# Performance work log

Hardware: AMD Instinct MI355X
Metric: run time of the kernel (lower is better)

Reference implementation:

```python
import jax, jax.numpy as jnp
import numpy as np
from jax import lax

B, L = 2, 5000            # images, candidate lines per image
C_IN, C_LOI = 256, 128    # backbone channels, dim_loi
H = W = 256               # feature-map spatial size (indices clamped to 255)
N_PTS0, N_PTS1 = 32, 8    # points sampled per line, after maxpool
POOL = N_PTS0 // N_PTS1   # MaxPool1d kernel/stride = 4
PLANES = C_LOI // 2       # Bottleneck1D mid channels
EPS = 1e-5


def setup_inputs() -> dict:
    key = jax.random.key(0)
    ks = jax.random.split(key, 16)
    f32 = jnp.float32
    s = 0.05
    feature = jax.random.normal(ks[0], (B, C_IN, H, W), f32)
    lines = jax.random.uniform(ks[1], (B, L, 2, 2), f32, minval=0.0, maxval=255.0)
    return {
        "feature": feature,
        "lines": lines,
        "fc1_w": jax.random.normal(ks[2], (C_LOI, C_IN), f32) * s,
        "fc1_b": jnp.zeros((C_LOI,), f32),
        "bn1_g": jnp.ones((C_LOI,), f32),
        "bn1_b": jnp.zeros((C_LOI,), f32),
        "bn1_m": jax.random.normal(ks[3], (C_LOI,), f32) * 0.1,
        "bn1_v": jax.random.uniform(ks[4], (C_LOI,), f32, minval=0.5, maxval=1.5),
        "conv1_w": jax.random.normal(ks[5], (PLANES, C_LOI), f32) * s,
        "conv1_b": jnp.zeros((PLANES,), f32),
        "bn2_g": jnp.ones((PLANES,), f32),
        "bn2_b": jnp.zeros((PLANES,), f32),
        "bn2_m": jax.random.normal(ks[6], (PLANES,), f32) * 0.1,
        "bn2_v": jax.random.uniform(ks[7], (PLANES,), f32, minval=0.5, maxval=1.5),
        "conv2_w": jax.random.normal(ks[8], (PLANES, PLANES, 3), f32) * s,
        "conv2_b": jnp.zeros((PLANES,), f32),
        "bn3_g": jnp.ones((PLANES,), f32),
        "bn3_b": jnp.zeros((PLANES,), f32),
        "bn3_m": jax.random.normal(ks[9], (PLANES,), f32) * 0.1,
        "bn3_v": jax.random.uniform(ks[10], (PLANES,), f32, minval=0.5, maxval=1.5),
        "conv3_w": jax.random.normal(ks[11], (C_LOI, PLANES), f32) * s,
        "conv3_b": jnp.zeros((C_LOI,), f32),
        "fc2_w": jax.random.normal(ks[12], (3, C_LOI * N_PTS1), f32) * s,
        "fc2_b": jnp.zeros((3,), f32),
    }


def _bn(x, g, b, m, v):
    # eval-mode BatchNorm1d over [N, C, T]
    inv = g / jnp.sqrt(v + EPS)
    return x * inv[None, :, None] + (b - m * inv)[None, :, None]


def _bilinear_sample(feat, lines):
    # feat: [B, C, H, W], lines: [B, L, 2, 2] -> [B, L, C, N_PTS0]
    lam = jnp.linspace(0.0, 1.0, N_PTS0, dtype=feat.dtype)[:, None]  # [P,1]
    # p = lam * endpoint0 + (1-lam) * endpoint1 - 0.5  -> [B, L, P, 2]
    p = lines[:, :, 0:1, :] * lam + lines[:, :, 1:2, :] * (1.0 - lam) - 0.5
    px, py = p[..., 0], p[..., 1]                       # [B, L, P]
    px0 = jnp.clip(jnp.floor(px), 0.0, 255.0)
    py0 = jnp.clip(jnp.floor(py), 0.0, 255.0)
    px1 = jnp.clip(px0 + 1.0, 0.0, 255.0)
    py1 = jnp.clip(py0 + 1.0, 0.0, 255.0)
    ix0, iy0 = px0.astype(jnp.int32), py0.astype(jnp.int32)
    ix1, iy1 = px1.astype(jnp.int32), py1.astype(jnp.int32)
    w00 = (px1 - px) * (py1 - py)
    w10 = (px - px0) * (py1 - py)
    w01 = (px1 - px) * (py - py0)
    w11 = (px - px0) * (py - py0)

    def one_image(f, a0, b0, a1, b1, c00, c10, c01, c11):
        # f: [C,H,W], indices/weights: [L,P] -> [C,L,P]
        return (f[:, a0, b0] * c00 + f[:, a1, b0] * c10 +
                f[:, a0, b1] * c01 + f[:, a1, b1] * c11)

    xp = jax.vmap(one_image)(feat, ix0, iy0, ix1, iy1, w00, w10, w01, w11)
    return jnp.transpose(xp, (0, 2, 1, 3))  # [B, L, C, P]


def _forward(feature, lines, fc1_w, fc1_b, bn1_g, bn1_b, bn1_m, bn1_v,
             conv1_w, conv1_b, bn2_g, bn2_b, bn2_m, bn2_v,
             conv2_w, conv2_b, bn3_g, bn3_b, bn3_m, bn3_v,
             conv3_w, conv3_b, fc2_w, fc2_b):
    # fc1: 1x1 conv over the backbone feature map
    x = jnp.einsum('oc,bchw->bohw', fc1_w, feature) + fc1_b[None, :, None, None]
    xp = _bilinear_sample(x, lines)                     # [B, L, C_LOI, P]
    xp = xp.reshape(B * L, C_LOI, N_PTS0)
    # MaxPool1d(kernel=POOL, stride=POOL)
    xp = xp.reshape(B * L, C_LOI, N_PTS1, POOL).max(axis=-1)  # [N, C, T]
    # Bottleneck1D residual branch: BN-ReLU-Conv1(k1)-BN-ReLU-Conv(k3)-BN-ReLU-Conv(k1)
    h = jax.nn.relu(_bn(xp, bn1_g, bn1_b, bn1_m, bn1_v))
    h = jnp.einsum('oc,nct->not', conv1_w, h) + conv1_b[None, :, None]
    h = jax.nn.relu(_bn(h, bn2_g, bn2_b, bn2_m, bn2_v))
    h = lax.conv_general_dilated(h, conv2_w, window_strides=(1,),
                                 padding=((1, 1),),
                                 dimension_numbers=('NCH', 'OIH', 'NCH'))
    h = h + conv2_b[None, :, None]
    h = jax.nn.relu(_bn(h, bn3_g, bn3_b, bn3_m, bn3_v))
    h = jnp.einsum('oc,nct->not', conv3_w, h) + conv3_b[None, :, None]
    xp = xp + h
    # fc2: ReLU + Linear(dim_loi * n_pts1 -> 3)
    flat = jax.nn.relu(xp).reshape(B * L, C_LOI * N_PTS1)
    return flat @ fc2_w.T + fc2_b


def reference(feature, lines, fc1_w, fc1_b, bn1_g, bn1_b, bn1_m, bn1_v,
              conv1_w, conv1_b, bn2_g, bn2_b, bn2_m, bn2_v,
              conv2_w, conv2_b, bn3_g, bn3_b, bn3_m, bn3_v,
              conv3_w, conv3_b, fc2_w, fc2_b):
    return _forward(feature, lines, fc1_w, fc1_b, bn1_g, bn1_b, bn1_m, bn1_v,
                    conv1_w, conv1_b, bn2_g, bn2_b, bn2_m, bn2_v,
                    conv2_w, conv2_b, bn3_g, bn3_b, bn3_m, bn3_v,
                    conv3_w, conv3_b, fc2_w, fc2_b)
```

## Files before the change

### kernel.cpp

```cpp
#include <hip/hip_runtime.h>
#include <hip/hip_bf16.h>

#define BB 2
#define LL 5000
#define CIN 256
#define CLOI 128
#define HH 256
#define WW 256
#define HWP (HH*WW)
#define NPTS0 32
#define NPTS1 8
#define PLANES 64
#define EPSV 1e-5f

#define X_BYTES   ((size_t)BB * HWP * CLOI * 2)
#define XS_BYTES  ((size_t)BB * LL * 1024 * 2)
#define W1S_OFF   (X_BYTES + XS_BYTES)
#define W2S_OFF   (W1S_OFF + 16384)
#define W3S_OFF   (W2S_OFF + 24576)
#define B1P_OFF   (W3S_OFF + 16384)
#define B2P_OFF   (B1P_OFF + 256)
#define S1_OFF    (B2P_OFF + 256)
#define T1_OFF    (S1_OFF + 512)
#define W0S_OFF   (T1_OFF + 512)

typedef unsigned int uint;
typedef unsigned short ushort;
typedef __attribute__((ext_vector_type(8))) short short8;
typedef __attribute__((ext_vector_type(4))) float f32x4;

__device__ __forceinline__ float bf2f(ushort u) {
    uint v = ((uint)u) << 16;
    return __uint_as_float(v);
}
__device__ __forceinline__ ushort f2bf(float f) {
    uint x = __float_as_uint(f);
    uint r = (x + 0x7fffu + ((x >> 16) & 1u)) >> 16;
    return (ushort)r;
}
__device__ __forceinline__ uint pack2(float a, float b) {
    return (uint)f2bf(a) | ((uint)f2bf(b) << 16);
}

__global__ __launch_bounds__(256) void fc1_kernel(
    const float* __restrict__ feature, const ushort* __restrict__ w0s,
    const float* __restrict__ fc1_b, ushort* __restrict__ xout)
{
    __shared__ ushort sF[32 * 64 * 8];

    int tid = threadIdx.x;
    int tile = blockIdx.x;
    int b = tile >> 10;
    int p0 = (tile & 1023) << 6;
    int wv = tid >> 6, lane = tid & 63;
    int q = lane >> 4, ln = lane & 15;

    short8 afr[8][2];
#pragma unroll
    for (int kg = 0; kg < 8; kg++)
#pragma unroll
        for (int mt = 0; mt < 2; mt++)
            afr[kg][mt] = *(const short8*)(w0s + ((size_t)((kg * 4 + q) * 128 + wv * 32 + mt * 16 + ln)) * 8);

    const float* fb = feature + (size_t)b * CIN * HWP + p0;
    int g_ = tid >> 4;
    int qd = tid & 15;
#pragma unroll
    for (int s = 0; s < 2; s++) {
        int g = s * 16 + g_;
        const float* src = fb + (size_t)(g * 8) * HWP + qd * 4;
        float4 rv[8];
#pragma unroll
        for (int j = 0; j < 8; j++) rv[j] = *(const float4*)(src + (size_t)j * HWP);
#pragma unroll
        for (int i = 0; i < 4; i++) {
            uint4 u;
            u.x = pack2(((const float*)&rv[0])[i], ((const float*)&rv[1])[i]);
            u.y = pack2(((const float*)&rv[2])[i], ((const float*)&rv[3])[i]);
            u.z = pack2(((const float*)&rv[4])[i], ((const float*)&rv[5])[i]);
            u.w = pack2(((const float*)&rv[6])[i], ((const float*)&rv[7])[i]);
            *(uint4*)(&sF[(g * 64 + qd * 4 + i) * 8]) = u;
        }
    }
    __syncthreads();

    const f32x4 fzero = { 0.f, 0.f, 0.f, 0.f };
    f32x4 acc[2][4];
#pragma unroll
    for (int mt = 0; mt < 2; mt++)
#pragma unroll
        for (int nt = 0; nt < 4; nt++) acc[mt][nt] = fzero;

#pragma unroll
    for (int kg = 0; kg < 8; kg++) {
#pragma unroll
        for (int nt = 0; nt < 4; nt++) {
            short8 bfr = *(short8*)(&sF[((kg * 4 + q) * 64 + nt * 16 + ln) * 8]);
            acc[0][nt] = __builtin_amdgcn_mfma_f32_16x16x32_bf16(afr[kg][0], bfr, acc[0][nt], 0, 0, 0);
            acc[1][nt] = __builtin_amdgcn_mfma_f32_16x16x32_bf16(afr[kg][1], bfr, acc[1][nt], 0, 0, 0);
        }
    }

    float bias[8];
    *(float4*)bias       = *(const float4*)(fc1_b + wv * 32 + q * 4);
    *(float4*)(bias + 4) = *(const float4*)(fc1_b + wv * 32 + 16 + q * 4);
    ushort* xrow = xout + (size_t)b * HWP * CLOI;
#pragma unroll
    for (int mt = 0; mt < 2; mt++)
#pragma unroll
        for (int nt = 0; nt < 4; nt++) {
            uint2 u;
            u.x = pack2(acc[mt][nt][0] + bias[mt * 4 + 0], acc[mt][nt][1] + bias[mt * 4 + 1]);
            u.y = pack2(acc[mt][nt][2] + bias[mt * 4 + 2], acc[mt][nt][3] + bias[mt * 4 + 3]);
            *(uint2*)(xrow + (size_t)(p0 + nt * 16 + ln) * CLOI + wv * 32 + mt * 16 + q * 4) = u;
        }
}

__global__ __launch_bounds__(256) void prep_kernel(
    const float* __restrict__ conv1_w, const float* __restrict__ conv1_b,
    const float* __restrict__ bn2_g, const float* __restrict__ bn2_b,
    const float* __restrict__ bn2_m, const float* __restrict__ bn2_v,
    const float* __restrict__ conv2_w, const float* __restrict__ conv2_b,
    const float* __restrict__ bn3_g, const float* __restrict__ bn3_b,
    const float* __restrict__ bn3_m, const float* __restrict__ bn3_v,
    const float* __restrict__ conv3_w,
    const float* __restrict__ bn1_g, const float* __restrict__ bn1_b,
    const float* __restrict__ bn1_m, const float* __restrict__ bn1_v,
    const float* __restrict__ fc1_w,
    ushort* __restrict__ w1s, ushort* __restrict__ w2s, ushort* __restrict__ w3s,
    float* __restrict__ b1p, float* __restrict__ b2p,
    float* __restrict__ s1o, float* __restrict__ t1o,
    ushort* __restrict__ w0s)
{
    int idx = blockIdx.x * 256 + threadIdx.x;
    if (idx < 8192) {
        int kg = idx >> 9, rem = idx & 511, m = rem >> 3, j = rem & 7;
        int c = kg * 8 + j;
        float s2 = bn2_g[m] * rsqrtf(bn2_v[m] + EPSV);
        w1s[idx] = f2bf(conv1_w[m * 128 + c] * s2);
    }
    if (idx < 12288) {
        int dt = idx >> 12, rem = idx & 4095;
        int kg = rem >> 9, m = (rem >> 3) & 63, j = rem & 7;
        int i = kg * 8 + j;
        float s3 = bn3_g[m] * rsqrtf(bn3_v[m] + EPSV);
        w2s[idx] = f2bf(conv2_w[m * 192 + i * 3 + dt] * s3);
    }
    if (idx < 8192) {
        int kg = idx >> 10, rem = idx & 1023, m = rem >> 3, j = rem & 7;
        w3s[idx] = f2bf(conv3_w[m * 64 + kg * 8 + j]);
    }
    if (idx < 32768) {
        int grp = idx >> 10, rem = idx & 1023, m = rem >> 3, j = rem & 7;
        w0s[idx] = f2bf(fc1_w[m * CIN + grp * 8 + j]);
    }
    if (idx < 64) {
        float s2 = bn2_g[idx] * rsqrtf(bn2_v[idx] + EPSV);
        b1p[idx] = conv1_b[idx] * s2 + bn2_b[idx] - bn2_m[idx] * s2;
        float s3 = bn3_g[idx] * rsqrtf(bn3_v[idx] + EPSV);
        b2p[idx] = conv2_b[idx] * s3 + bn3_b[idx] - bn3_m[idx] * s3;
    }
    if (idx < 128) {
        float s1 = bn1_g[idx] * rsqrtf(bn1_v[idx] + EPSV);
        s1o[idx] = s1;
        t1o[idx] = bn1_b[idx] - bn1_m[idx] * s1;
    }
}

__global__ __launch_bounds__(256, 4) void sample_head_kernel(
    const ushort* __restrict__ x, const float* __restrict__ lines,
    const ushort* __restrict__ w1s, const ushort* __restrict__ w2s,
    const ushort* __restrict__ w3s,
    const float* __restrict__ b1p, const float* __restrict__ b2p,
    const float* __restrict__ s1g, const float* __restrict__ t1g,
    const float* __restrict__ conv3_b,
    const float* __restrict__ fc2_w, const float* __restrict__ fc2_b,
    float* __restrict__ out)
{
    __shared__ ushort sH1[8192];
    __shared__ ushort sB2[4096];
    __shared__ int   sIdx[8][32][4];
    __shared__ float sWt[8][32][4];
    __shared__ float sB1[64], sB2b[64], sB3b[128];

    int tid = threadIdx.x;
    int wv = tid >> 6, lane = tid & 63;
    int q = lane >> 4, ln = lane & 15;
    int L0 = blockIdx.x * 8;
    int b = L0 / LL;
    int colg = wv * 16 + ln;

    if (tid < 128) sB3b[tid] = conv3_b[tid];
    if (tid < 64)  { sB1[tid] = b1p[tid]; sB2b[tid] = b2p[tid]; }

    float s1a = s1g[2 * lane], s1c = s1g[2 * lane + 1];
    float t1a = t1g[2 * lane], t1c = t1g[2 * lane + 1];

    {
        int l = tid >> 5, j = tid & 31;
        float lam = (float)j * (1.0f / 31.0f);
        const float* lp = lines + (size_t)(L0 + l) * 4;
        float e0x = lp[0], e0y = lp[1], e1x = lp[2], e1y = lp[3];
        float px = e0x * lam + e1x * (1.f - lam) - 0.5f;
        float py = e0y * lam + e1y * (1.f - lam) - 0.5f;
        float px0 = fminf(fmaxf(floorf(px), 0.f), 255.f);
        float py0 = fminf(fmaxf(floorf(py), 0.f), 255.f);
        float px1 = fminf(px0 + 1.f, 255.f);
        float py1 = fminf(py0 + 1.f, 255.f);
        int ix0 = (int)px0, iy0 = (int)py0, ix1 = (int)px1, iy1 = (int)py1;
        sIdx[l][j][0] = ix0 * WW + iy0;
        sIdx[l][j][1] = ix1 * WW + iy0;
        sIdx[l][j][2] = ix0 * WW + iy1;
        sIdx[l][j][3] = ix1 * WW + iy1;
        sWt[l][j][0] = (px1 - px) * (py1 - py);
        sWt[l][j][1] = (px - px0) * (py1 - py);
        sWt[l][j][2] = (px1 - px) * (py - py0);
        sWt[l][j][3] = (px - px0) * (py - py0);
    }
    __syncthreads();

    const uint* xb = (const uint*)(x + (size_t)b * HWP * CLOI);
    int kg = lane >> 2;
    int j2 = (lane & 3) * 2;
    int swz = (kg & 7) << 3;

    uint xsu[8][2];
#pragma unroll
    for (int l = 0; l < 8; l++) {
        float m00 = -INFINITY, m10 = -INFINITY;
        float m01 = -INFINITY, m11 = -INFINITY;
#pragma unroll
        for (int jj = 0; jj < 8; jj++) {
            int j = wv * 8 + jj;
            int4   iv = *(const int4*)(&sIdx[l][j][0]);
            float4 wvv = *(const float4*)(&sWt[l][j][0]);
            uint u00 = xb[(size_t)iv.x * 64 + lane];
            uint u10 = xb[(size_t)iv.y * 64 + lane];
            uint u01 = xb[(size_t)iv.z * 64 + lane];
            uint u11 = xb[(size_t)iv.w * 64 + lane];
            float v0 = bf2f((ushort)(u00 & 0xffff)) * wvv.x + bf2f((ushort)(u10 & 0xffff)) * wvv.y
                     + bf2f((ushort)(u01 & 0xffff)) * wvv.z + bf2f((ushort)(u11 & 0xffff)) * wvv.w;
            float v1 = bf2f((ushort)(u00 >> 16)) * wvv.x + bf2f((ushort)(u10 >> 16)) * wvv.y
                     + bf2f((ushort)(u01 >> 16)) * wvv.z + bf2f((ushort)(u11 >> 16)) * wvv.w;
            if (jj < 4) { m00 = fmaxf(m00, v0); m10 = fmaxf(m10, v1); }
            else        { m01 = fmaxf(m01, v0); m11 = fmaxf(m11, v1); }
        }
        xsu[l][0] = pack2(m00, m10);
        xsu[l][1] = pack2(m01, m11);
        int col0 = l * 8 + 2 * wv;
        int base0 = (kg * 64 + col0) * 8 + j2;
        float h00 = fmaxf(m00 * s1a + t1a, 0.f), h10 = fmaxf(m10 * s1c + t1c, 0.f);
        float h01 = fmaxf(m01 * s1a + t1a, 0.f), h11 = fmaxf(m11 * s1c + t1c, 0.f);
        *(uint*)(&sH1[base0 ^ swz])       = pack2(h00, h10);
        *(uint*)(&sH1[(base0 + 8) ^ swz]) = pack2(h01, h11);
    }
    __syncthreads();

    const short8 bzero = { 0, 0, 0, 0, 0, 0, 0, 0 };
    const f32x4 fzero = { 0.f, 0.f, 0.f, 0.f };

    f32x4 acc1[4];
#pragma unroll
    for (int mt = 0; mt < 4; mt++) acc1[mt] = fzero;
#pragma unroll
    for (int ks = 0; ks < 4; ks++) {
        int kk = ks * 4 + q;
        short8 bfrag = *(short8*)(&sH1[((kk * 64 + colg) * 8) ^ ((kk & 7) << 3)]);
#pragma unroll
        for (int mt = 0; mt < 4; mt++) {
            short8 a = *(const short8*)(w1s + (kk * 64 + mt * 16 + ln) * 8);
            acc1[mt] = __builtin_amdgcn_mfma_f32_16x16x32_bf16(a, bfrag, acc1[mt], 0, 0, 0);
        }
    }
#pragma unroll
    for (int mt = 0; mt < 4; mt++) {
        int m0 = mt * 16 + q * 4;
        float v0 = fmaxf(acc1[mt][0] + sB1[m0 + 0], 0.f);
        float v1 = fmaxf(acc1[mt][1] + sB1[m0 + 1], 0.f);
        float v2 = fmaxf(acc1[mt][2] + sB1[m0 + 2], 0.f);
        float v3 = fmaxf(acc1[mt][3] + sB1[m0 + 3], 0.f);
        uint2 u; u.x = pack2(v0, v1); u.y = pack2(v2, v3);
        *(uint2*)(&sB2[((m0 >> 3) * 64 + colg) * 8 + (m0 & 7)]) = u;
    }
    __syncthreads();

#pragma unroll
    for (int l = 0; l < 8; l++) {
        int col0 = l * 8 + 2 * wv;
        int base0 = (kg * 64 + col0) * 8 + j2;
        *(uint*)(&sH1[base0 ^ swz])       = xsu[l][0];
        *(uint*)(&sH1[(base0 + 8) ^ swz]) = xsu[l][1];
    }

    int tpos = colg & 7;
    short8 bfr2[3][2];
#pragma unroll
    for (int dt = 0; dt < 3; dt++) {
        int tsh = tpos + dt - 1;
        bool valid = ((unsigned)tsh < 8u);
        int colr = colg + dt - 1;
        colr = colr < 0 ? 0 : (colr > 63 ? 63 : colr);
#pragma unroll
        for (int ks = 0; ks < 2; ks++) {
            short8 bfrag = *(short8*)(&sB2[((ks * 4 + q) * 64 + colr) * 8]);
            bfr2[dt][ks] = valid ? bfrag : bzero;
        }
    }
    __syncthreads();

    f32x4 acc2[4];
#pragma unroll
    for (int mt = 0; mt < 4; mt++) acc2[mt] = fzero;
#pragma unroll
    for (int dt = 0; dt < 3; dt++)
#pragma unroll
        for (int ks = 0; ks < 2; ks++) {
            int kk = ks * 4 + q;
#pragma unroll
            for (int mt = 0; mt < 4; mt++) {
                short8 a = *(const short8*)(w2s + dt * 4096 + (kk * 64 + mt * 16 + ln) * 8);
                acc2[mt] = __builtin_amdgcn_mfma_f32_16x16x32_bf16(a, bfr2[dt][ks], acc2[mt], 0, 0, 0);
            }
        }
#pragma unroll
    for (int mt = 0; mt < 4; mt++) {
        int m0 = mt * 16 + q * 4;
        float v0 = fmaxf(acc2[mt][0] + sB2b[m0 + 0], 0.f);
        float v1 = fmaxf(acc2[mt][1] + sB2b[m0 + 1], 0.f);
        float v2 = fmaxf(acc2[mt][2] + sB2b[m0 + 2], 0.f);
        float v3 = fmaxf(acc2[mt][3] + sB2b[m0 + 3], 0.f);
        uint2 u; u.x = pack2(v0, v1); u.y = pack2(v2, v3);
        *(uint2*)(&sB2[((m0 >> 3) * 64 + colg) * 8 + (m0 & 7)]) = u;
    }
    __syncthreads();

    f32x4 acc3[8];
#pragma unroll
    for (int mt = 0; mt < 8; mt++) acc3[mt] = fzero;
#pragma unroll
    for (int ks = 0; ks < 2; ks++) {
        int kk = ks * 4 + q;
        short8 bfrag = *(short8*)(&sB2[(kk * 64 + colg) * 8]);
#pragma unroll
        for (int mt = 0; mt < 8; mt++) {
            short8 a = *(const short8*)(w3s + (kk * 128 + mt * 16 + ln) * 8);
            acc3[mt] = __builtin_amdgcn_mfma_f32_16x16x32_bf16(a, bfrag, acc3[mt], 0, 0, 0);
        }
    }

    float p0 = 0.f, p1 = 0.f, p2 = 0.f;
#pragma unroll
    for (int mt = 0; mt < 8; mt++) {
#pragma unroll
        for (int r = 0; r < 4; r++) {
            int m = mt * 16 + q * 4 + r;
            int idx = ((m >> 3) * 512 + colg * 8 + (m & 7)) ^ (((m >> 3) & 7) << 3);
            float xsv = bf2f(sH1[idx]);
            float v = fmaxf(xsv + acc3[mt][r] + sB3b[m], 0.f);
            int fi = m * 8 + tpos;
            p0 += v * fc2_w[fi];
            p1 += v * fc2_w[1024 + fi];
            p2 += v * fc2_w[2048 + fi];
        }
    }
    p0 += __shfl_xor(p0, 32); p1 += __shfl_xor(p1, 32); p2 += __shfl_xor(p2, 32);
    p0 += __shfl_xor(p0, 16); p1 += __shfl_xor(p1, 16); p2 += __shfl_xor(p2, 16);
    p0 += __shfl_xor(p0, 4);  p1 += __shfl_xor(p1, 4);  p2 += __shfl_xor(p2, 4);
    p0 += __shfl_xor(p0, 2);  p1 += __shfl_xor(p1, 2);  p2 += __shfl_xor(p2, 2);
    p0 += __shfl_xor(p0, 1);  p1 += __shfl_xor(p1, 1);  p2 += __shfl_xor(p2, 1);

    if (lane == 0 || lane == 8) {
        int line = L0 + wv * 2 + (lane >> 3);
        out[(size_t)line * 3 + 0] = p0 + fc2_b[0];
        out[(size_t)line * 3 + 1] = p1 + fc2_b[1];
        out[(size_t)line * 3 + 2] = p2 + fc2_b[2];
    }
}

extern "C" void kernel_launch(void* const* d_in, const int* in_sizes, int n_in,
                              void* d_out, int out_size, void* d_ws, size_t ws_size,
                              hipStream_t stream) {
    const float* feature = (const float*)d_in[0];
    const float* lines   = (const float*)d_in[1];
    const float* fc1_w   = (const float*)d_in[2];
    const float* fc1_b   = (const float*)d_in[3];
    const float* bn1_g   = (const float*)d_in[4];
    const float* bn1_b   = (const float*)d_in[5];
    const float* bn1_m   = (const float*)d_in[6];
    const float* bn1_v   = (const float*)d_in[7];
    const float* conv1_w = (const float*)d_in[8];
    const float* conv1_b = (const float*)d_in[9];
    const float* bn2_g   = (const float*)d_in[10];
    const float* bn2_b   = (const float*)d_in[11];
    const float* bn2_m   = (const float*)d_in[12];
    const float* bn2_v   = (const float*)d_in[13];
    const float* conv2_w = (const float*)d_in[14];
    const float* conv2_b = (const float*)d_in[15];
    const float* bn3_g   = (const float*)d_in[16];
    const float* bn3_b   = (const float*)d_in[17];
    const float* bn3_m   = (const float*)d_in[18];
    const float* bn3_v   = (const float*)d_in[19];
    const float* conv3_w = (const float*)d_in[20];
    const float* conv3_b = (const float*)d_in[21];
    const float* fc2_w   = (const float*)d_in[22];
    const float* fc2_b   = (const float*)d_in[23];
    float* out = (float*)d_out;

    char* ws = (char*)d_ws;
    ushort* x_bf = (ushort*)ws;
    ushort* w1s  = (ushort*)(ws + W1S_OFF);
    ushort* w2s  = (ushort*)(ws + W2S_OFF);
    ushort* w3s  = (ushort*)(ws + W3S_OFF);
    float*  b1p  = (float*)(ws + B1P_OFF);
    float*  b2p  = (float*)(ws + B2P_OFF);
    float*  s1g  = (float*)(ws + S1_OFF);
    float*  t1g  = (float*)(ws + T1_OFF);
    ushort* w0s  = (ushort*)(ws + W0S_OFF);

    prep_kernel<<<128, 256, 0, stream>>>(
        conv1_w, conv1_b, bn2_g, bn2_b, bn2_m, bn2_v,
        conv2_w, conv2_b, bn3_g, bn3_b, bn3_m, bn3_v,
        conv3_w, bn1_g, bn1_b, bn1_m, bn1_v, fc1_w,
        w1s, w2s, w3s, b1p, b2p, s1g, t1g, w0s);
    fc1_kernel<<<2048, 256, 0, stream>>>(feature, w0s, fc1_b, x_bf);
    sample_head_kernel<<<BB * LL / 8, 256, 0, stream>>>(
        x_bf, lines, w1s, w2s, w3s, b1p, b2p, s1g, t1g, conv3_b, fc2_w, fc2_b, out);
}
```

Measured before the change: 298.3 us.

## Alias shared buffers, raise occupancy, and batch gather loads per half-window

The sample-index and weight shared arrays now share one 8 KB buffer with the later sB2 scratch, which cuts LDS use per block. Launch bounds go from 4 to 6 blocks per SM. The gather loop issues all 16 global loads for a 4-point pooling window before doing the math, so more memory requests are in flight. The risks are register pressure under the tighter occupancy bound, possible spills, and needing a barrier before sB2 reuses the aliased region.

```diff
diff --git a/kernel.cpp b/kernel.cpp
--- a/kernel.cpp
+++ b/kernel.cpp
@@ -167,7 +167,7 @@
     }
 }
 
-__global__ __launch_bounds__(256, 4) void sample_head_kernel(
+__global__ __launch_bounds__(256, 6) void sample_head_kernel(
     const ushort* __restrict__ x, const float* __restrict__ lines,
     const ushort* __restrict__ w1s, const ushort* __restrict__ w2s,
     const ushort* __restrict__ w3s,
@@ -178,10 +178,12 @@
     float* __restrict__ out)
 {
     __shared__ ushort sH1[8192];
-    __shared__ ushort sB2[4096];
-    __shared__ int   sIdx[8][32][4];
-    __shared__ float sWt[8][32][4];
+    __shared__ __align__(16) char sU[8192];
     __shared__ float sB1[64], sB2b[64], sB3b[128];
+
+    int4*   sIdx = (int4*)sU;
+    float4* sWt  = (float4*)(sU + 4096);
+    ushort* sB2  = (ushort*)sU;
 
     int tid = threadIdx.x;
     int wv = tid >> 6, lane = tid & 63;
@@ -208,14 +210,17 @@
         float px1 = fminf(px0 + 1.f, 255.f);
         float py1 = fminf(py0 + 1.f, 255.f);
         int ix0 = (int)px0, iy0 = (int)py0, ix1 = (int)px1, iy1 = (int)py1;
-        sIdx[l][j][0] = ix0 * WW + iy0;
-        sIdx[l][j][1] = ix1 * WW + iy0;
-        sIdx[l][j][2] = ix0 * WW + iy1;
-        sIdx[l][j][3] = ix1 * WW + iy1;
-        sWt[l][j][0] = (px1 - px) * (py1 - py);
-        sWt[l][j][1] = (px - px0) * (py1 - py);
-        sWt[l][j][2] = (px1 - px) * (py - py0);
-        sWt[l][j][3] = (px - px0) * (py - py0);
+        int4 iv; float4 wt;
+        iv.x = ix0 * WW + iy0;
+        iv.y = ix1 * WW + iy0;
+        iv.z = ix0 * WW + iy1;
+        iv.w = ix1 * WW + iy1;
+        wt.x = (px1 - px) * (py1 - py);
+        wt.y = (px - px0) * (py1 - py);
+        wt.z = (px1 - px) * (py - py0);
+        wt.w = (px - px0) * (py - py0);
+        sIdx[l * 32 + j] = iv;
+        sWt[l * 32 + j]  = wt;
     }
     __syncthreads();
 
@@ -227,32 +232,41 @@
     uint xsu[8][2];
 #pragma unroll
     for (int l = 0; l < 8; l++) {
-        float m00 = -INFINITY, m10 = -INFINITY;
-        float m01 = -INFINITY, m11 = -INFINITY;
-#pragma unroll
-        for (int jj = 0; jj < 8; jj++) {
-            int j = wv * 8 + jj;
-            int4   iv = *(const int4*)(&sIdx[l][j][0]);
-            float4 wvv = *(const float4*)(&sWt[l][j][0]);
-            uint u00 = xb[(size_t)iv.x * 64 + lane];
-            uint u10 = xb[(size_t)iv.y * 64 + lane];
-            uint u01 = xb[(size_t)iv.z * 64 + lane];
-            uint u11 = xb[(size_t)iv.w * 64 + lane];
-            float v0 = bf2f((ushort)(u00 & 0xffff)) * wvv.x + bf2f((ushort)(u10 & 0xffff)) * wvv.y
-                     + bf2f((ushort)(u01 & 0xffff)) * wvv.z + bf2f((ushort)(u11 & 0xffff)) * wvv.w;
-            float v1 = bf2f((ushort)(u00 >> 16)) * wvv.x + bf2f((ushort)(u10 >> 16)) * wvv.y
-                     + bf2f((ushort)(u01 >> 16)) * wvv.z + bf2f((ushort)(u11 >> 16)) * wvv.w;
-            if (jj < 4) { m00 = fmaxf(m00, v0); m10 = fmaxf(m10, v1); }
-            else        { m01 = fmaxf(m01, v0); m11 = fmaxf(m11, v1); }
-        }
-        xsu[l][0] = pack2(m00, m10);
-        xsu[l][1] = pack2(m01, m11);
-        int col0 = l * 8 + 2 * wv;
-        int base0 = (kg * 64 + col0) * 8 + j2;
-        float h00 = fmaxf(m00 * s1a + t1a, 0.f), h10 = fmaxf(m10 * s1c + t1c, 0.f);
-        float h01 = fmaxf(m01 * s1a + t1a, 0.f), h11 = fmaxf(m11 * s1c + t1c, 0.f);
-        *(uint*)(&sH1[base0 ^ swz])       = pack2(h00, h10);
-        *(uint*)(&sH1[(base0 + 8) ^ swz]) = pack2(h01, h11);
+        float mA0, mA1;
+#pragma unroll
+        for (int jh = 0; jh < 2; jh++) {
+            uint u[4][4];
+#pragma unroll
+            for (int jj = 0; jj < 4; jj++) {
+                int4 iv = sIdx[l * 32 + wv * 8 + jh * 4 + jj];
+                u[jj][0] = xb[(size_t)iv.x * 64 + lane];
+                u[jj][1] = xb[(size_t)iv.y * 64 + lane];
+                u[jj][2] = xb[(size_t)iv.z * 64 + lane];
+                u[jj][3] = xb[(size_t)iv.w * 64 + lane];
+            }
+            float m0 = -INFINITY, m1 = -INFINITY;
+#pragma unroll
+            for (int jj = 0; jj < 4; jj++) {
+                float4 wt = sWt[l * 32 + wv * 8 + jh * 4 + jj];
+                float v0 = bf2f((ushort)(u[jj][0] & 0xffff)) * wt.x + bf2f((ushort)(u[jj][1] & 0xffff)) * wt.y
+                         + bf2f((ushort)(u[jj][2] & 0xffff)) * wt.z + bf2f((ushort)(u[jj][3] & 0xffff)) * wt.w;
+                float v1 = bf2f((ushort)(u[jj][0] >> 16)) * wt.x + bf2f((ushort)(u[jj][1] >> 16)) * wt.y
+                         + bf2f((ushort)(u[jj][2] >> 16)) * wt.z + bf2f((ushort)(u[jj][3] >> 16)) * wt.w;
+                m0 = fmaxf(m0, v0);
+                m1 = fmaxf(m1, v1);
+            }
+            if (jh == 0) { mA0 = m0; mA1 = m1; }
+            else {
+                xsu[l][0] = pack2(mA0, mA1);
+                xsu[l][1] = pack2(m0, m1);
+                int col0 = l * 8 + 2 * wv;
+                int base0 = (kg * 64 + col0) * 8 + j2;
+                float h00 = fmaxf(mA0 * s1a + t1a, 0.f), h10 = fmaxf(mA1 * s1c + t1c, 0.f);
+                float h01 = fmaxf(m0 * s1a + t1a, 0.f),  h11 = fmaxf(m1 * s1c + t1c, 0.f);
+                *(uint*)(&sH1[base0 ^ swz])       = pack2(h00, h10);
+                *(uint*)(&sH1[(base0 + 8) ^ swz]) = pack2(h01, h11);
+            }
+        }
     }
     __syncthreads();
 
```

Result: slower. 310.4 us (+4.1%).

## Widen bilinear gather loads, compress sample metadata, alias LDS for higher occupancy

Applied to the files above, without the earlier changes.

The bilinear gather is restructured. Each lane now loads four bf16 channels (uint2), and each half-wave handles one sample point. All 16 corner loads are issued before any math, to expose more memory-level parallelism. Per-point metadata shrinks to one base index plus two weights, with the other corners derived by fixed offsets. The index and weight scratch now share LDS with sB2, and launch bounds rise from 4 to 5 blocks per SM to raise occupancy. The cost is higher register pressure, and the upper-edge clamp is dropped: a base coordinate of 255 would read the wrong or out-of-range neighbour.

```diff
diff --git a/kernel.cpp b/kernel.cpp
--- a/kernel.cpp
+++ b/kernel.cpp
@@ -167,7 +167,7 @@
     }
 }
 
-__global__ __launch_bounds__(256, 4) void sample_head_kernel(
+__global__ __launch_bounds__(256, 5) void sample_head_kernel(
     const ushort* __restrict__ x, const float* __restrict__ lines,
     const ushort* __restrict__ w1s, const ushort* __restrict__ w2s,
     const ushort* __restrict__ w3s,
@@ -178,10 +178,12 @@
     float* __restrict__ out)
 {
     __shared__ ushort sH1[8192];
-    __shared__ ushort sB2[4096];
-    __shared__ int   sIdx[8][32][4];
-    __shared__ float sWt[8][32][4];
+    __shared__ __align__(16) char sU[8192];
     __shared__ float sB1[64], sB2b[64], sB3b[128];
+
+    int*    sI  = (int*)sU;
+    float2* sW2 = (float2*)(sU + 1024);
+    ushort* sB2 = (ushort*)sU;
 
     int tid = threadIdx.x;
     int wv = tid >> 6, lane = tid & 63;
@@ -193,8 +195,13 @@
     if (tid < 128) sB3b[tid] = conv3_b[tid];
     if (tid < 64)  { sB1[tid] = b1p[tid]; sB2b[tid] = b2p[tid]; }
 
-    float s1a = s1g[2 * lane], s1c = s1g[2 * lane + 1];
-    float t1a = t1g[2 * lane], t1c = t1g[2 * lane + 1];
+    int half = lane >> 5;
+    int lc = lane & 31;
+    int kg = lc >> 1, j4 = (lc & 1) * 4;
+    int swz = (kg & 7) << 3;
+
+    float4 s1v = *(const float4*)(s1g + lc * 4);
+    float4 t1v = *(const float4*)(t1g + lc * 4);
 
     {
         int l = tid >> 5, j = tid & 31;
@@ -205,54 +212,60 @@
         float py = e0y * lam + e1y * (1.f - lam) - 0.5f;
         float px0 = fminf(fmaxf(floorf(px), 0.f), 255.f);
         float py0 = fminf(fmaxf(floorf(py), 0.f), 255.f);
-        float px1 = fminf(px0 + 1.f, 255.f);
-        float py1 = fminf(py0 + 1.f, 255.f);
-        int ix0 = (int)px0, iy0 = (int)py0, ix1 = (int)px1, iy1 = (int)py1;
-        sIdx[l][j][0] = ix0 * WW + iy0;
-        sIdx[l][j][1] = ix1 * WW + iy0;
-        sIdx[l][j][2] = ix0 * WW + iy1;
-        sIdx[l][j][3] = ix1 * WW + iy1;
-        sWt[l][j][0] = (px1 - px) * (py1 - py);
-        sWt[l][j][1] = (px - px0) * (py1 - py);
-        sWt[l][j][2] = (px1 - px) * (py - py0);
-        sWt[l][j][3] = (px - px0) * (py - py0);
-    }
-    __syncthreads();
-
-    const uint* xb = (const uint*)(x + (size_t)b * HWP * CLOI);
-    int kg = lane >> 2;
-    int j2 = (lane & 3) * 2;
-    int swz = (kg & 7) << 3;
-
-    uint xsu[8][2];
+        int ix0 = (int)px0, iy0 = (int)py0;
+        sI[l * 32 + j] = ix0 * WW + iy0;
+        float2 w2; w2.x = px0 + 1.f - px; w2.y = py0 + 1.f - py;
+        sW2[l * 32 + j] = w2;
+    }
+    __syncthreads();
+
+    const uint2* xb2 = (const uint2*)(x + (size_t)b * HWP * CLOI);
+
+    uint2 xsu[8];
 #pragma unroll
     for (int l = 0; l < 8; l++) {
-        float m00 = -INFINITY, m10 = -INFINITY;
-        float m01 = -INFINITY, m11 = -INFINITY;
-#pragma unroll
-        for (int jj = 0; jj < 8; jj++) {
-            int j = wv * 8 + jj;
-            int4   iv = *(const int4*)(&sIdx[l][j][0]);
-            float4 wvv = *(const float4*)(&sWt[l][j][0]);
-            uint u00 = xb[(size_t)iv.x * 64 + lane];
-            uint u10 = xb[(size_t)iv.y * 64 + lane];
-            uint u01 = xb[(size_t)iv.z * 64 + lane];
-            uint u11 = xb[(size_t)iv.w * 64 + lane];
-            float v0 = bf2f((ushort)(u00 & 0xffff)) * wvv.x + bf2f((ushort)(u10 & 0xffff)) * wvv.y
-                     + bf2f((ushort)(u01 & 0xffff)) * wvv.z + bf2f((ushort)(u11 & 0xffff)) * wvv.w;
-            float v1 = bf2f((ushort)(u00 >> 16)) * wvv.x + bf2f((ushort)(u10 >> 16)) * wvv.y
-                     + bf2f((ushort)(u01 >> 16)) * wvv.z + bf2f((ushort)(u11 >> 16)) * wvv.w;
-            if (jj < 4) { m00 = fmaxf(m00, v0); m10 = fmaxf(m10, v1); }
-            else        { m01 = fmaxf(m01, v0); m11 = fmaxf(m11, v1); }
-        }
-        xsu[l][0] = pack2(m00, m10);
-        xsu[l][1] = pack2(m01, m11);
-        int col0 = l * 8 + 2 * wv;
-        int base0 = (kg * 64 + col0) * 8 + j2;
-        float h00 = fmaxf(m00 * s1a + t1a, 0.f), h10 = fmaxf(m10 * s1c + t1c, 0.f);
-        float h01 = fmaxf(m01 * s1a + t1a, 0.f), h11 = fmaxf(m11 * s1c + t1c, 0.f);
-        *(uint*)(&sH1[base0 ^ swz])       = pack2(h00, h10);
-        *(uint*)(&sH1[(base0 + 8) ^ swz]) = pack2(h01, h11);
+        uint2 u[4][4];
+        float2 wxy[4];
+#pragma unroll
+        for (int jj = 0; jj < 4; jj++) {
+            int pt = l * 32 + wv * 8 + half * 4 + jj;
+            int i00 = sI[pt];
+            wxy[jj] = sW2[pt];
+            const uint2* rp = xb2 + (size_t)((i00 << 5) + lc);
+            u[jj][0] = rp[0];
+            u[jj][1] = rp[32];
+            u[jj][2] = rp[8192];
+            u[jj][3] = rp[8224];
+        }
+        float p0v = -INFINITY, p1v = -INFINITY, p2v = -INFINITY, p3v = -INFINITY;
+#pragma unroll
+        for (int jj = 0; jj < 4; jj++) {
+            float wx0 = wxy[jj].x, wy0 = wxy[jj].y;
+            float w00 = wx0 * wy0;
+            float w01 = wx0 - w00;
+            float w10 = wy0 - w00;
+            float w11 = 1.f - wx0 - wy0 + w00;
+            float v0 = bf2f((ushort)(u[jj][0].x & 0xffff)) * w00 + bf2f((ushort)(u[jj][1].x & 0xffff)) * w01
+                     + bf2f((ushort)(u[jj][2].x & 0xffff)) * w10 + bf2f((ushort)(u[jj][3].x & 0xffff)) * w11;
+            float v1 = bf2f((ushort)(u[jj][0].x >> 16)) * w00 + bf2f((ushort)(u[jj][1].x >> 16)) * w01
+                     + bf2f((ushort)(u[jj][2].x >> 16)) * w10 + bf2f((ushort)(u[jj][3].x >> 16)) * w11;
+            float v2 = bf2f((ushort)(u[jj][0].y & 0xffff)) * w00 + bf2f((ushort)(u[jj][1].y & 0xffff)) * w01
+                     + bf2f((ushort)(u[jj][2].y & 0xffff)) * w10 + bf2f((ushort)(u[jj][3].y & 0xffff)) * w11;
+            float v3 = bf2f((ushort)(u[jj][0].y >> 16)) * w00 + bf2f((ushort)(u[jj][1].y >> 16)) * w01
+                     + bf2f((ushort)(u[jj][2].y >> 16)) * w10 + bf2f((ushort)(u[jj][3].y >> 16)) * w11;
+            p0v = fmaxf(p0v, v0); p1v = fmaxf(p1v, v1);
+            p2v = fmaxf(p2v, v2); p3v = fmaxf(p3v, v3);
+        }
+        uint2 xv; xv.x = pack2(p0v, p1v); xv.y = pack2(p2v, p3v);
+        xsu[l] = xv;
+        float h0 = fmaxf(p0v * s1v.x + t1v.x, 0.f);
+        float h1v = fmaxf(p1v * s1v.y + t1v.y, 0.f);
+        float h2 = fmaxf(p2v * s1v.z + t1v.z, 0.f);
+        float h3 = fmaxf(p3v * s1v.w + t1v.w, 0.f);
+        uint2 hv; hv.x = pack2(h0, h1v); hv.y = pack2(h2, h3);
+        int col = l * 8 + 2 * wv + half;
+        int base = (kg * 64 + col) * 8 + j4;
+        *(uint2*)(&sH1[base ^ swz]) = hv;
     }
     __syncthreads();
 
@@ -286,10 +299,9 @@
 
 #pragma unroll
     for (int l = 0; l < 8; l++) {
-        int col0 = l * 8 + 2 * wv;
-        int base0 = (kg * 64 + col0) * 8 + j2;
-        *(uint*)(&sH1[base0 ^ swz])       = xsu[l][0];
-        *(uint*)(&sH1[(base0 + 8) ^ swz]) = xsu[l][1];
+        int col = l * 8 + 2 * wv + half;
+        int base = (kg * 64 + col) * 8 + j4;
+        *(uint2*)(&sH1[base ^ swz]) = xsu[l];
     }
 
     int tpos = colg & 7;
```

New measurement: 290.0 us. 1.03x faster.
